# Kernel tuning notes

Measured on AMD Instinct MI355X. Metric: run time of the kernel, lower is better.

## Reference

```python
import jax, jax.numpy as jnp
import numpy as np

B, S, D, H = 4, 2048, 768, 3072

def _layernorm(X):
    # manual LayerNorm: biased variance, no eps, no affine
    mu = jnp.mean(X, axis=2, keepdims=True)
    sigma = jnp.sqrt(jnp.mean(jnp.square(X - mu), axis=2, keepdims=True))
    return (X - mu) / sigma

def setup_inputs() -> dict:
    key = jax.random.key(0)
    ks = jax.random.split(key, 11)
    sc = 0.02
    return {
        "X": jax.random.normal(ks[0], (B, S, D), dtype=jnp.float32),
        "Wq": jax.random.normal(ks[1], (D, D), dtype=jnp.float32) * sc,
        "bq": jnp.zeros((D,), dtype=jnp.float32),
        "Wk": jax.random.normal(ks[2], (D, D), dtype=jnp.float32) * sc,
        "bk": jnp.zeros((D,), dtype=jnp.float32),
        "Wv": jax.random.normal(ks[3], (D, D), dtype=jnp.float32) * sc,
        "bv": jnp.zeros((D,), dtype=jnp.float32),
        "W1": jax.random.normal(ks[4], (D, H), dtype=jnp.float32) * sc,
        "b1": jnp.zeros((H,), dtype=jnp.float32),
        "W2": jax.random.normal(ks[5], (H, D), dtype=jnp.float32) * sc,
        "b2": jnp.zeros((D,), dtype=jnp.float32),
    }

def reference(X, Wq, bq, Wk, bk, Wv, bv, W1, b1, W2, b2):
    dk = jnp.sqrt(jnp.asarray(X.shape[2], dtype=X.dtype))
    Q = X @ Wq + bq
    K = X @ Wk + bk
    V = X @ Wv + bv
    A = jnp.einsum('bqd,bkd->bqk', Q, K)
    # faithful: tril zeroes (not -inf) above-diagonal BEFORE softmax
    A = jnp.tril(A) / dk
    A = jax.nn.softmax(A, axis=2)
    # faithful to einsum 'ijk,ijl->ijl': sum A over k, broadcast onto V
    AV = jnp.sum(A, axis=2, keepdims=True) * V
    X = _layernorm(X + AV)
    F = jax.nn.relu(X @ W1 + b1) @ W2 + b2
    X = _layernorm(X + F)
    return X
```

## Files before the change

kernel.cpp:

```cpp
#include <hip/hip_runtime.h>
#include <hip/hip_bf16.h>
#include <math.h>


typedef __bf16 bf16x8 __attribute__((ext_vector_type(8)));
typedef float f32x4 __attribute__((ext_vector_type(4)));

__device__ inline void gload_lds16(const __hip_bfloat16* g, void* lds) {
  __builtin_amdgcn_global_load_lds(
      (const __attribute__((address_space(1))) void*)g,
      (__attribute__((address_space(3))) void*)lds, 16, 0, 0);
}

__device__ inline float bf2f(unsigned short u) {
  union { unsigned int i; float f; } x;
  x.i = ((unsigned int)u) << 16;
  return x.f;
}

#define BARRIER() asm volatile("s_barrier" ::: "memory")

template <int BNv, int EPI>
__global__ __launch_bounds__(256, 2) void gemm128(
    const __hip_bfloat16* __restrict__ A, const __hip_bfloat16* __restrict__ Bt,
    __hip_bfloat16* __restrict__ C, const float* __restrict__ bias,
    const float* __restrict__ residf, const __hip_bfloat16* __restrict__ residb,
    int M, int N, int K) {
  constexpr int NF = BNv / 32;
  constexpr int BI = BNv / 32;
  constexpr int BS = BNv * 128;
  __shared__ __align__(16) char smem[32768 + 2 * BS];

  const int bid = blockIdx.x;
  const int mB = M / 128;
  const int rowBase = (bid % mB) * 128;
  const int colBase = (bid / mB) * BNv;
  const int nt = K / 64;

  const int wv = threadIdx.x >> 6;
  const int lane = threadIdx.x & 63;
  const int wr = wv >> 1, wc = wv & 1;
  const int l16 = lane & 15, lk = lane >> 4;

  const int rA = lane >> 3;
  const int cSw = ((lane & 7) ^ rA) * 8;
  const __hip_bfloat16* gA = A + (size_t)(rowBase + wv * 32 + rA) * K + cSw;
  const __hip_bfloat16* gB =
      Bt + (size_t)(colBase + wv * 8 * BI + rA) * K + cSw;

  auto STAGE = [&](int kt, int b) {
    const size_t ko = (size_t)kt * 64;
#pragma unroll
    for (int i = 0; i < 4; ++i)
      gload_lds16(gA + (size_t)i * 8 * K + ko,
                  smem + b * 16384 + (wv * 4 + i) * 1024);
#pragma unroll
    for (int i = 0; i < BI; ++i)
      gload_lds16(gB + (size_t)i * 8 * K + ko,
                  smem + 32768 + b * BS + (wv * BI + i) * 1024);
  };

  const int aBase = (wr * 64 + l16) * 128;
  const int bBase = (wc * (BNv / 2) + l16) * 128;
  const int xr = l16 & 7;
  const int cph0 = ((lk) ^ xr) * 16;
  const int cph1 = ((4 + lk) ^ xr) * 16;

  f32x4 acc[4][NF];
#pragma unroll
  for (int m = 0; m < 4; ++m)
#pragma unroll
    for (int n = 0; n < NF; ++n) acc[m][n] = (f32x4){0.f, 0.f, 0.f, 0.f};

  STAGE(0, 0);
  if (nt > 1) {
    STAGE(1, 1);
    if constexpr (BNv == 128)
      asm volatile("s_waitcnt vmcnt(8)" ::: "memory");
    else
      asm volatile("s_waitcnt vmcnt(7)" ::: "memory");
  } else {
    asm volatile("s_waitcnt vmcnt(0)" ::: "memory");
  }
  BARRIER();

  for (int t = 0; t < nt; ++t) {
    const int b = t & 1;
    const char* pa = smem + b * 16384 + aBase;
    const char* pb = smem + 32768 + b * BS + bBase;

    bf16x8 af0[4], af1[4], bf0[NF], bf1[NF];
#pragma unroll
    for (int m = 0; m < 4; ++m) af0[m] = *(const bf16x8*)(pa + m * 2048 + cph0);
#pragma unroll
    for (int n = 0; n < NF; ++n) bf0[n] = *(const bf16x8*)(pb + n * 2048 + cph0);
#pragma unroll
    for (int m = 0; m < 4; ++m) af1[m] = *(const bf16x8*)(pa + m * 2048 + cph1);
#pragma unroll
    for (int n = 0; n < NF; ++n) bf1[n] = *(const bf16x8*)(pb + n * 2048 + cph1);

    if constexpr (NF == 4)
      asm volatile("s_waitcnt lgkmcnt(8)" ::: "memory");
    else
      asm volatile("s_waitcnt lgkmcnt(7)" ::: "memory");
    __builtin_amdgcn_sched_barrier(0);
    __builtin_amdgcn_s_setprio(1);
#pragma unroll
    for (int m = 0; m < 4; ++m)
#pragma unroll
      for (int n = 0; n < NF; ++n)
        acc[m][n] = __builtin_amdgcn_mfma_f32_16x16x32_bf16(af0[m], bf0[n],
                                                            acc[m][n], 0, 0, 0);
    __builtin_amdgcn_s_setprio(0);
    asm volatile("s_waitcnt lgkmcnt(0)" ::: "memory");
    __builtin_amdgcn_sched_barrier(0);
    BARRIER();

    if (t + 2 < nt) STAGE(t + 2, b);

    __builtin_amdgcn_s_setprio(1);
#pragma unroll
    for (int m = 0; m < 4; ++m)
#pragma unroll
      for (int n = 0; n < NF; ++n)
        acc[m][n] = __builtin_amdgcn_mfma_f32_16x16x32_bf16(af1[m], bf1[n],
                                                            acc[m][n], 0, 0, 0);
    __builtin_amdgcn_s_setprio(0);

    if (t + 1 < nt) {
      if (t + 2 < nt) {
        if constexpr (BNv == 128)
          asm volatile("s_waitcnt vmcnt(8)" ::: "memory");
        else
          asm volatile("s_waitcnt vmcnt(7)" ::: "memory");
      } else {
        asm volatile("s_waitcnt vmcnt(0)" ::: "memory");
      }
      BARRIER();
    }
  }

#pragma unroll
  for (int m = 0; m < 4; ++m) {
#pragma unroll
    for (int n = 0; n < NF; ++n) {
#pragma unroll
      for (int j = 0; j < 4; ++j) {
        const int r = rowBase + wr * 64 + m * 16 + lk * 4 + j;
        const int c = colBase + wc * (BNv / 2) + n * 16 + l16;
        const size_t idx = (size_t)r * N + c;
        float v = acc[m][n][j] + bias[c];
        if (EPI == 1) v += residf[idx];
        if (EPI == 2) v = fmaxf(v, 0.f);
        if (EPI == 3) v += __bfloat162float(residb[idx]);
        C[idx] = __float2bfloat16(v);
      }
    }
  }
}

template <bool OUTF>
__global__ __launch_bounds__(256) void ln_simple(
    const __hip_bfloat16* __restrict__ Y, __hip_bfloat16* __restrict__ outb,
    float* __restrict__ outf) {
  const int wave = threadIdx.x >> 6, lane = threadIdx.x & 63;
  const size_t base = ((size_t)blockIdx.x * 4 + wave) * 768;

  float v[12];
  float s = 0.f, q = 0.f;
#pragma unroll
  for (int c = 0; c < 3; ++c) {
    const int col = c * 256 + lane * 4;
    ushort4 a = *reinterpret_cast<const ushort4*>(&Y[base + col]);
    float y0 = bf2f(a.x), y1 = bf2f(a.y), y2 = bf2f(a.z), y3 = bf2f(a.w);
    v[c * 4 + 0] = y0; v[c * 4 + 1] = y1; v[c * 4 + 2] = y2; v[c * 4 + 3] = y3;
    s += y0 + y1 + y2 + y3;
    q += y0 * y0 + y1 * y1 + y2 * y2 + y3 * y3;
  }
#pragma unroll
  for (int off = 32; off; off >>= 1) {
    s += __shfl_xor(s, off);
    q += __shfl_xor(q, off);
  }
  const float mu = s * (1.f / 768.f);
  const float rs = rsqrtf(q * (1.f / 768.f) - mu * mu);
#pragma unroll
  for (int c = 0; c < 3; ++c) {
    const int col = c * 256 + lane * 4;
    if (OUTF) {
      float4 o;
      o.x = (v[c * 4 + 0] - mu) * rs;
      o.y = (v[c * 4 + 1] - mu) * rs;
      o.z = (v[c * 4 + 2] - mu) * rs;
      o.w = (v[c * 4 + 3] - mu) * rs;
      *reinterpret_cast<float4*>(&outf[base + col]) = o;
    } else {
      __hip_bfloat16 h0 = __float2bfloat16((v[c * 4 + 0] - mu) * rs);
      __hip_bfloat16 h1 = __float2bfloat16((v[c * 4 + 1] - mu) * rs);
      __hip_bfloat16 h2 = __float2bfloat16((v[c * 4 + 2] - mu) * rs);
      __hip_bfloat16 h3 = __float2bfloat16((v[c * 4 + 3] - mu) * rs);
      ushort4 o;
      o.x = *reinterpret_cast<unsigned short*>(&h0);
      o.y = *reinterpret_cast<unsigned short*>(&h1);
      o.z = *reinterpret_cast<unsigned short*>(&h2);
      o.w = *reinterpret_cast<unsigned short*>(&h3);
      *reinterpret_cast<ushort4*>(&outb[base + col]) = o;
    }
  }
}

__device__ inline void tc_tile(const float* __restrict__ W,
                               __hip_bfloat16* __restrict__ Wt, int K, int N,
                               int n0, int k0, int t) {
  __shared__ float tile[32][33];
  const int tx = t & 31;
  const int ty = t >> 5;
#pragma unroll
  for (int i = 0; i < 32; i += 8)
    tile[ty + i][tx] = W[(size_t)(k0 + ty + i) * N + n0 + tx];
  __syncthreads();
#pragma unroll
  for (int i = 0; i < 32; i += 8)
    Wt[(size_t)(n0 + ty + i) * K + k0 + tx] = __float2bfloat16(tile[tx][ty + i]);
}

__global__ __launch_bounds__(256) void prep_kernel(
    const float* __restrict__ X, const float* __restrict__ Wv,
    const float* __restrict__ W1, const float* __restrict__ W2,
    __hip_bfloat16* __restrict__ Xb, __hip_bfloat16* __restrict__ Wvt,
    __hip_bfloat16* __restrict__ W1t, __hip_bfloat16* __restrict__ W2t) {
  const int bid = blockIdx.x;
  const int t = threadIdx.x;
  if (bid < 6144) {
    const int i = bid * 256 + t;
    float4 v = reinterpret_cast<const float4*>(X)[i];
    __hip_bfloat16 h0 = __float2bfloat16(v.x), h1 = __float2bfloat16(v.y);
    __hip_bfloat16 h2 = __float2bfloat16(v.z), h3 = __float2bfloat16(v.w);
    ushort4 o;
    o.x = *reinterpret_cast<unsigned short*>(&h0);
    o.y = *reinterpret_cast<unsigned short*>(&h1);
    o.z = *reinterpret_cast<unsigned short*>(&h2);
    o.w = *reinterpret_cast<unsigned short*>(&h3);
    reinterpret_cast<ushort4*>(Xb)[i] = o;
  } else if (bid < 6720) {
    const int idx = bid - 6144;
    tc_tile(Wv, Wvt, 768, 768, (idx % 24) * 32, (idx / 24) * 32, t);
  } else if (bid < 9024) {
    const int idx = bid - 6720;
    tc_tile(W1, W1t, 768, 3072, (idx % 96) * 32, (idx / 96) * 32, t);
  } else {
    const int idx = bid - 9024;
    tc_tile(W2, W2t, 3072, 768, (idx % 24) * 32, (idx / 24) * 32, t);
  }
}

extern "C" void kernel_launch(void* const* d_in, const int* in_sizes, int n_in,
                              void* d_out, int out_size, void* d_ws,
                              size_t ws_size, hipStream_t stream) {
  const float* X = (const float*)d_in[0];
  const float* Wv = (const float*)d_in[5];
  const float* bv = (const float*)d_in[6];
  const float* W1 = (const float*)d_in[7];
  const float* b1 = (const float*)d_in[8];
  const float* W2 = (const float*)d_in[9];
  const float* b2 = (const float*)d_in[10];
  float* out = (float*)d_out;

  const int M = 4 * 2048;
  const int D = 768, H = 3072;

  char* ws = (char*)d_ws;
  __hip_bfloat16* Xb  = (__hip_bfloat16*)(ws);
  __hip_bfloat16* Wvt = (__hip_bfloat16*)(ws + 12582912);
  __hip_bfloat16* W1t = (__hip_bfloat16*)(ws + 13762560);
  __hip_bfloat16* W2t = (__hip_bfloat16*)(ws + 18481152);
  __hip_bfloat16* Yb  = (__hip_bfloat16*)(ws + 23199744);
  __hip_bfloat16* X1b = (__hip_bfloat16*)(ws + 35782656);
  __hip_bfloat16* Gb  = (__hip_bfloat16*)(ws + 48365568);
  __hip_bfloat16* Y2b = Yb;

  prep_kernel<<<11328, 256, 0, stream>>>(X, Wv, W1, W2, Xb, Wvt, W1t, W2t);

  gemm128<96, 1><<<512, 256, 0, stream>>>(Xb, Wvt, Yb, bv, X, nullptr, M, D, D);
  ln_simple<false><<<M / 4, 256, 0, stream>>>(Yb, X1b, nullptr);
  gemm128<128, 2><<<1536, 256, 0, stream>>>(X1b, W1t, Gb, b1, nullptr, nullptr,
                                            M, H, D);
  gemm128<96, 3><<<512, 256, 0, stream>>>(Gb, W2t, Y2b, b2, nullptr, X1b, M, D,
                                          H);
  ln_simple<true><<<M / 4, 256, 0, stream>>>(Y2b, nullptr, out);
}
```

Measured before the change: 125.3 us.

## Switch GEMM mainloop to 4-stage BK=32 ring with register double-buffered fragments

Restructures the bf16 MFMA GEMM mainloop. K tiles shrink from 64 to 32, and LDS becomes a 4-buffer ring with three tiles prefetched ahead. Each iteration loads the next tile's fragments into alternate registers while MFMAs run on the current ones, with one barrier per step instead of two. The aim is to hide global and LDS latency behind compute, at the cost of twice as many iterations and barriers, new swizzle and waitcnt bookkeeping, and an assumption that nt is even and at least 3.

```diff
diff --git a/kernel.cpp b/kernel.cpp
--- a/kernel.cpp
+++ b/kernel.cpp
@@ -27,44 +27,56 @@
     const float* __restrict__ residf, const __hip_bfloat16* __restrict__ residb,
     int M, int N, int K) {
   constexpr int NF = BNv / 32;
-  constexpr int BI = BNv / 32;
-  constexpr int BS = BNv * 128;
-  __shared__ __align__(16) char smem[32768 + 2 * BS];
+  constexpr int BS2 = BNv * 64;
+  __shared__ __align__(16) char smem[32768 + 4 * BS2];
 
   const int bid = blockIdx.x;
   const int mB = M / 128;
   const int rowBase = (bid % mB) * 128;
   const int colBase = (bid / mB) * BNv;
-  const int nt = K / 64;
+  const int nt = K / 32;
 
   const int wv = threadIdx.x >> 6;
   const int lane = threadIdx.x & 63;
   const int wr = wv >> 1, wc = wv & 1;
   const int l16 = lane & 15, lk = lane >> 4;
-
-  const int rA = lane >> 3;
-  const int cSw = ((lane & 7) ^ rA) * 8;
-  const __hip_bfloat16* gA = A + (size_t)(rowBase + wv * 32 + rA) * K + cSw;
-  const __hip_bfloat16* gB =
-      Bt + (size_t)(colBase + wv * 8 * BI + rA) * K + cSw;
+  const bool hasB = (BNv == 128) || (wv < 3);
+  const bool SW4 = hasB;
+
+  const int sr = lane >> 2;
+  const int scol = ((lane & 3) ^ ((sr >> 1) & 3)) * 8;
+  const __hip_bfloat16* gA = A + (size_t)(rowBase + wv * 32 + sr) * K + scol;
+  const __hip_bfloat16* gB = Bt + (size_t)(colBase + wv * 32 + sr) * K + scol;
 
   auto STAGE = [&](int kt, int b) {
-    const size_t ko = (size_t)kt * 64;
-#pragma unroll
-    for (int i = 0; i < 4; ++i)
-      gload_lds16(gA + (size_t)i * 8 * K + ko,
-                  smem + b * 16384 + (wv * 4 + i) * 1024);
-#pragma unroll
-    for (int i = 0; i < BI; ++i)
-      gload_lds16(gB + (size_t)i * 8 * K + ko,
-                  smem + 32768 + b * BS + (wv * BI + i) * 1024);
+    const size_t ko = (size_t)kt * 32;
+#pragma unroll
+    for (int i = 0; i < 2; ++i)
+      gload_lds16(gA + (size_t)i * 16 * K + ko,
+                  smem + b * 8192 + (wv * 2 + i) * 1024);
+    if (hasB) {
+#pragma unroll
+      for (int i = 0; i < 2; ++i)
+        gload_lds16(gB + (size_t)i * 16 * K + ko,
+                    smem + 32768 + b * BS2 + (wv * 2 + i) * 1024);
+    }
   };
 
-  const int aBase = (wr * 64 + l16) * 128;
-  const int bBase = (wc * (BNv / 2) + l16) * 128;
-  const int xr = l16 & 7;
-  const int cph0 = ((lk) ^ xr) * 16;
-  const int cph1 = ((4 + lk) ^ xr) * 16;
+  auto WAITSTAGE = [&](int t) {
+    if (t + 3 < nt) {
+      if (SW4) asm volatile("s_waitcnt vmcnt(8)" ::: "memory");
+      else     asm volatile("s_waitcnt vmcnt(4)" ::: "memory");
+    } else if (t + 2 < nt) {
+      if (SW4) asm volatile("s_waitcnt vmcnt(4)" ::: "memory");
+      else     asm volatile("s_waitcnt vmcnt(2)" ::: "memory");
+    } else {
+      asm volatile("s_waitcnt vmcnt(0)" ::: "memory");
+    }
+  };
+
+  const int aByte = (wr * 64 + l16) * 64;
+  const int bByte = (wc * (BNv / 2) + l16) * 64;
+  const int cph = (lk ^ ((l16 >> 1) & 3)) * 16;
 
   f32x4 acc[4][NF];
 #pragma unroll
@@ -72,73 +84,59 @@
 #pragma unroll
     for (int n = 0; n < NF; ++n) acc[m][n] = (f32x4){0.f, 0.f, 0.f, 0.f};
 
+  bf16x8 a0[4], b0[NF], a1[4], b1[NF];
+
   STAGE(0, 0);
-  if (nt > 1) {
-    STAGE(1, 1);
-    if constexpr (BNv == 128)
-      asm volatile("s_waitcnt vmcnt(8)" ::: "memory");
-    else
-      asm volatile("s_waitcnt vmcnt(7)" ::: "memory");
-  } else {
-    asm volatile("s_waitcnt vmcnt(0)" ::: "memory");
-  }
+  STAGE(1, 1);
+  STAGE(2, 2);
+  if (SW4) asm volatile("s_waitcnt vmcnt(8)" ::: "memory");
+  else     asm volatile("s_waitcnt vmcnt(4)" ::: "memory");
   BARRIER();
-
-  for (int t = 0; t < nt; ++t) {
-    const int b = t & 1;
-    const char* pa = smem + b * 16384 + aBase;
-    const char* pb = smem + 32768 + b * BS + bBase;
-
-    bf16x8 af0[4], af1[4], bf0[NF], bf1[NF];
-#pragma unroll
-    for (int m = 0; m < 4; ++m) af0[m] = *(const bf16x8*)(pa + m * 2048 + cph0);
-#pragma unroll
-    for (int n = 0; n < NF; ++n) bf0[n] = *(const bf16x8*)(pb + n * 2048 + cph0);
-#pragma unroll
-    for (int m = 0; m < 4; ++m) af1[m] = *(const bf16x8*)(pa + m * 2048 + cph1);
-#pragma unroll
-    for (int n = 0; n < NF; ++n) bf1[n] = *(const bf16x8*)(pb + n * 2048 + cph1);
-
-    if constexpr (NF == 4)
-      asm volatile("s_waitcnt lgkmcnt(8)" ::: "memory");
-    else
-      asm volatile("s_waitcnt lgkmcnt(7)" ::: "memory");
-    __builtin_amdgcn_sched_barrier(0);
-    __builtin_amdgcn_s_setprio(1);
-#pragma unroll
-    for (int m = 0; m < 4; ++m)
-#pragma unroll
-      for (int n = 0; n < NF; ++n)
-        acc[m][n] = __builtin_amdgcn_mfma_f32_16x16x32_bf16(af0[m], bf0[n],
-                                                            acc[m][n], 0, 0, 0);
-    __builtin_amdgcn_s_setprio(0);
-    asm volatile("s_waitcnt lgkmcnt(0)" ::: "memory");
-    __builtin_amdgcn_sched_barrier(0);
-    BARRIER();
-
-    if (t + 2 < nt) STAGE(t + 2, b);
-
-    __builtin_amdgcn_s_setprio(1);
-#pragma unroll
-    for (int m = 0; m < 4; ++m)
-#pragma unroll
-      for (int n = 0; n < NF; ++n)
-        acc[m][n] = __builtin_amdgcn_mfma_f32_16x16x32_bf16(af1[m], bf1[n],
-                                                            acc[m][n], 0, 0, 0);
-    __builtin_amdgcn_s_setprio(0);
-
-    if (t + 1 < nt) {
-      if (t + 2 < nt) {
-        if constexpr (BNv == 128)
-          asm volatile("s_waitcnt vmcnt(8)" ::: "memory");
-        else
-          asm volatile("s_waitcnt vmcnt(7)" ::: "memory");
-      } else {
-        asm volatile("s_waitcnt vmcnt(0)" ::: "memory");
-      }
-      BARRIER();
-    }
-  }
+  {
+    const char* pa = smem + aByte;
+    const char* pb = smem + 32768 + bByte;
+#pragma unroll
+    for (int m = 0; m < 4; ++m) a0[m] = *(const bf16x8*)(pa + m * 1024 + cph);
+#pragma unroll
+    for (int n = 0; n < NF; ++n) b0[n] = *(const bf16x8*)(pb + n * 1024 + cph);
+  }
+
+#define ITER(T, CA, CB, NA, NB)                                               \
+  {                                                                           \
+    const int t_ = (T);                                                       \
+    asm volatile("s_waitcnt lgkmcnt(0)" ::: "memory");                        \
+    __builtin_amdgcn_sched_barrier(0);                                        \
+    if (t_ + 3 < nt) STAGE(t_ + 3, (t_ + 3) & 3);                             \
+    WAITSTAGE(t_);                                                            \
+    BARRIER();                                                                \
+    if (t_ + 1 < nt) {                                                        \
+      const char* pa = smem + ((t_ + 1) & 3) * 8192 + aByte;                  \
+      const char* pb = smem + 32768 + ((t_ + 1) & 3) * BS2 + bByte;           \
+      _Pragma("unroll")                                                       \
+      for (int m = 0; m < 4; ++m)                                             \
+        NA[m] = *(const bf16x8*)(pa + m * 1024 + cph);                        \
+      _Pragma("unroll")                                                       \
+      for (int n = 0; n < NF; ++n)                                            \
+        NB[n] = *(const bf16x8*)(pb + n * 1024 + cph);                        \
+    }                                                                         \
+    __builtin_amdgcn_sched_barrier(0);                                        \
+    __builtin_amdgcn_s_setprio(1);                                            \
+    _Pragma("unroll")                                                         \
+    for (int m = 0; m < 4; ++m) {                                             \
+      _Pragma("unroll")                                                       \
+      for (int n = 0; n < NF; ++n)                                            \
+        acc[m][n] = __builtin_amdgcn_mfma_f32_16x16x32_bf16(CA[m], CB[n],     \
+                                                            acc[m][n], 0, 0,  \
+                                                            0);               \
+    }                                                                         \
+    __builtin_amdgcn_s_setprio(0);                                            \
+  }
+
+  for (int t = 0; t < nt; t += 2) {
+    ITER(t, a0, b0, a1, b1);
+    ITER(t + 1, a1, b1, a0, b0);
+  }
+#undef ITER
 
 #pragma unroll
   for (int m = 0; m < 4; ++m) {
```

Measured after the change: 148.7 us. 18.7% more time.

## Use 256x256 ping-pong GEMM for FFN with split-K second GEMM fused into final LN

Applied to the files above, without the earlier changes.

Adds a 512-thread 256x256-tile bf16 MFMA GEMM with a four-slot LDS pipeline and interleaved phase barriers. The FFN up-projection runs on it, and the down-projection runs on it as a split-K=2 kernel writing two bf16 partials. A new final LayerNorm kernel sums the partials, residual and bias. The larger tiles aim to raise data reuse and MFMA utilisation and to fill the GPU better for N=768. The cost is extra partial-sum traffic and an extra rounding of the partials to bf16. Workspace offsets are reshuffled so Gb and Yb alias.

```diff
diff --git a/kernel.cpp b/kernel.cpp
--- a/kernel.cpp
+++ b/kernel.cpp
@@ -19,6 +19,165 @@
 }
 
 #define BARRIER() asm volatile("s_barrier" ::: "memory")
+
+template <int EPI>
+__global__ __launch_bounds__(512, 2) void gemm256(
+    const __hip_bfloat16* __restrict__ A, const __hip_bfloat16* __restrict__ Bt,
+    __hip_bfloat16* __restrict__ C, const float* __restrict__ bias,
+    int M, int N, int K, int Ksub, int mB, int nB) {
+  __shared__ __align__(16) char smem[131072];
+
+  const int bid = blockIdx.x;
+  const int bpz = mB * nB;
+  const int z = bid / bpz;
+  const int rem = bid % bpz;
+  const int rowBase = (rem % mB) * 256;
+  const int colBase = (rem / mB) * 256;
+  const int kBase = z * Ksub;
+  const int nt = Ksub / 64;
+
+  const int wv = threadIdx.x >> 6;
+  const int lane = threadIdx.x & 63;
+  const int wr = wv >> 2;
+  const int wc = wv & 3;
+  const int l16 = lane & 15, lk = lane >> 4;
+
+  const int srow = lane >> 3;
+  const int scol = ((lane & 7) ^ srow) * 8;
+  const __hip_bfloat16* gA =
+      A + (size_t)(rowBase + srow) * K + kBase + scol;
+  const __hip_bfloat16* gB =
+      Bt + (size_t)(colBase + srow) * K + kBase + scol;
+
+  auto SA = [&](int tau, int h) {
+    if (tau >= 2 && tau < nt) {
+      const int slot = (2 * tau + h) & 3;
+#pragma unroll
+      for (int i = 0; i < 2; ++i)
+        gload_lds16(gA + (size_t)(128 * h + 8 * (2 * wv + i)) * K +
+                        (size_t)tau * 64,
+                    smem + slot * 16384 + (wv * 2 + i) * 1024);
+    }
+  };
+  auto SB = [&](int tau, int h) {
+    if (tau >= 2 && tau < nt) {
+      const int slot = (2 * tau + h) & 3;
+#pragma unroll
+      for (int i = 0; i < 2; ++i)
+        gload_lds16(gB + (size_t)(128 * h + 8 * (2 * wv + i)) * K +
+                        (size_t)tau * 64,
+                    smem + 65536 + slot * 16384 + (wv * 2 + i) * 1024);
+    }
+  };
+
+  const int aOff = l16 * 128;
+  const int bOff = (wc & 1) * 8192 + l16 * 128;
+  const int cph0 = ((lk) ^ (l16 & 7)) * 16;
+  const int cph1 = ((4 + lk) ^ (l16 & 7)) * 16;
+
+  f32x4 acc[8][4];
+#pragma unroll
+  for (int m = 0; m < 8; ++m)
+#pragma unroll
+    for (int n = 0; n < 4; ++n) acc[m][n] = (f32x4){0.f, 0.f, 0.f, 0.f};
+
+  bf16x8 bq0[4], bq1[4];
+
+  {
+#pragma unroll
+    for (int tt = 0; tt < 2; ++tt) {
+      const int s0 = 2 * tt;
+#pragma unroll
+      for (int h = 0; h < 2; ++h)
+#pragma unroll
+        for (int i = 0; i < 2; ++i)
+          gload_lds16(gA + (size_t)(128 * h + 8 * (2 * wv + i)) * K +
+                          (size_t)tt * 64,
+                      smem + (s0 + h) * 16384 + (wv * 2 + i) * 1024);
+#pragma unroll
+      for (int h = 0; h < 2; ++h)
+#pragma unroll
+        for (int i = 0; i < 2; ++i)
+          gload_lds16(gB + (size_t)(128 * h + 8 * (2 * wv + i)) * K +
+                          (size_t)tt * 64,
+                      smem + 65536 + (s0 + h) * 16384 + (wv * 2 + i) * 1024);
+    }
+    asm volatile("s_waitcnt vmcnt(8)" ::: "memory");
+    BARRIER();
+  }
+
+#define PH(T, MH, READB, BQ, CPH, STG, VM)                                   \
+  {                                                                          \
+    const char* pa_ = smem + (((2 * (T) + wr) & 3) * 16384) + aOff;          \
+    bf16x8 af_[4];                                                           \
+    _Pragma("unroll") for (int m_ = 0; m_ < 4; ++m_) af_[m_] =               \
+        *(const bf16x8*)(pa_ + ((MH)*4 + m_) * 2048 + (CPH));                \
+    if (READB) {                                                             \
+      const char* pb_ =                                                      \
+          smem + 65536 + (((2 * (T) + (wc >> 1)) & 3) * 16384) + bOff;       \
+      _Pragma("unroll") for (int n_ = 0; n_ < 4; ++n_) BQ[n_] =              \
+          *(const bf16x8*)(pb_ + n_ * 2048 + (CPH));                         \
+    }                                                                        \
+    STG;                                                                     \
+    BARRIER();                                                               \
+    asm volatile("s_waitcnt lgkmcnt(0)" ::: "memory");                       \
+    __builtin_amdgcn_sched_barrier(0);                                       \
+    __builtin_amdgcn_s_setprio(1);                                           \
+    _Pragma("unroll") for (int m_ = 0; m_ < 4; ++m_) {                       \
+      _Pragma("unroll") for (int n_ = 0; n_ < 4; ++n_) acc[(MH)*4 + m_][n_] =\
+          __builtin_amdgcn_mfma_f32_16x16x32_bf16(af_[m_], BQ[n_],           \
+                                                  acc[(MH)*4 + m_][n_], 0,   \
+                                                  0, 0);                     \
+    }                                                                        \
+    __builtin_amdgcn_s_setprio(0);                                           \
+    VM;                                                                      \
+    BARRIER();                                                               \
+  }
+
+  const int iters = nt / 2;
+  for (int i = 0; i < iters; ++i) {
+    const int e = 2 * i, o = 2 * i + 1;
+    PH(e, 0, 1, bq0, cph0, SB(o, 1), (void)0);
+    PH(e, 1, 0, bq0, cph0, SA(o, 0), (void)0);
+    PH(e, 0, 1, bq1, cph1, SA(o, 1), (void)0);
+    if (e + 2 < nt) {
+      PH(e, 1, 0, bq1, cph1, SB(e + 2, 0),
+         asm volatile("s_waitcnt vmcnt(2)" ::: "memory"));
+    } else {
+      PH(e, 1, 0, bq1, cph1, (void)0,
+         asm volatile("s_waitcnt vmcnt(0)" ::: "memory"));
+    }
+    if (e + 2 < nt) {
+      PH(o, 0, 1, bq0, cph0, SB(e + 2, 1), (void)0);
+      PH(o, 1, 0, bq0, cph0, SA(e + 2, 0), (void)0);
+      PH(o, 0, 1, bq1, cph1, SA(e + 2, 1), (void)0);
+      PH(o, 1, 0, bq1, cph1, SB(o + 2, 0),
+         asm volatile("s_waitcnt vmcnt(2)" ::: "memory"));
+    } else {
+      PH(o, 0, 1, bq0, cph0, (void)0, (void)0);
+      PH(o, 1, 0, bq0, cph0, (void)0, (void)0);
+      PH(o, 0, 1, bq1, cph1, (void)0, (void)0);
+      PH(o, 1, 0, bq1, cph1, (void)0, (void)0);
+    }
+  }
+#undef PH
+
+  __hip_bfloat16* Cz = C + (size_t)z * M * N;
+#pragma unroll
+  for (int m = 0; m < 8; ++m) {
+#pragma unroll
+    for (int n = 0; n < 4; ++n) {
+#pragma unroll
+      for (int j = 0; j < 4; ++j) {
+        const int r = rowBase + wr * 128 + m * 16 + lk * 4 + j;
+        const int c = colBase + wc * 64 + n * 16 + l16;
+        float v = acc[m][n][j];
+        if (EPI == 2) v = fmaxf(v + bias[c], 0.f);
+        Cz[(size_t)r * N + c] = __float2bfloat16(v);
+      }
+    }
+  }
+}
 
 template <int BNv, int EPI>
 __global__ __launch_bounds__(256, 2) void gemm128(
@@ -206,6 +365,49 @@
       o.w = *reinterpret_cast<unsigned short*>(&h3);
       *reinterpret_cast<ushort4*>(&outb[base + col]) = o;
     }
+  }
+}
+
+__global__ __launch_bounds__(256) void ln_fuse2_final(
+    const __hip_bfloat16* __restrict__ P0, const __hip_bfloat16* __restrict__ P1,
+    const __hip_bfloat16* __restrict__ residb, const float* __restrict__ bias,
+    float* __restrict__ outf) {
+  const int wave = threadIdx.x >> 6, lane = threadIdx.x & 63;
+  const size_t base = ((size_t)blockIdx.x * 4 + wave) * 768;
+
+  float v[12];
+  float s = 0.f, q = 0.f;
+#pragma unroll
+  for (int c = 0; c < 3; ++c) {
+    const int col = c * 256 + lane * 4;
+    ushort4 a = *reinterpret_cast<const ushort4*>(&P0[base + col]);
+    ushort4 b = *reinterpret_cast<const ushort4*>(&P1[base + col]);
+    ushort4 rb = *reinterpret_cast<const ushort4*>(&residb[base + col]);
+    float4 bs = *reinterpret_cast<const float4*>(&bias[col]);
+    float y0 = bf2f(a.x) + bf2f(b.x) + bf2f(rb.x) + bs.x;
+    float y1 = bf2f(a.y) + bf2f(b.y) + bf2f(rb.y) + bs.y;
+    float y2 = bf2f(a.z) + bf2f(b.z) + bf2f(rb.z) + bs.z;
+    float y3 = bf2f(a.w) + bf2f(b.w) + bf2f(rb.w) + bs.w;
+    v[c * 4 + 0] = y0; v[c * 4 + 1] = y1; v[c * 4 + 2] = y2; v[c * 4 + 3] = y3;
+    s += y0 + y1 + y2 + y3;
+    q += y0 * y0 + y1 * y1 + y2 * y2 + y3 * y3;
+  }
+#pragma unroll
+  for (int off = 32; off; off >>= 1) {
+    s += __shfl_xor(s, off);
+    q += __shfl_xor(q, off);
+  }
+  const float mu = s * (1.f / 768.f);
+  const float rs = rsqrtf(q * (1.f / 768.f) - mu * mu);
+#pragma unroll
+  for (int c = 0; c < 3; ++c) {
+    const int col = c * 256 + lane * 4;
+    float4 o;
+    o.x = (v[c * 4 + 0] - mu) * rs;
+    o.y = (v[c * 4 + 1] - mu) * rs;
+    o.z = (v[c * 4 + 2] - mu) * rs;
+    o.w = (v[c * 4 + 3] - mu) * rs;
+    *reinterpret_cast<float4*>(&outf[base + col]) = o;
   }
 }
 
@@ -273,19 +475,19 @@
   __hip_bfloat16* Xb  = (__hip_bfloat16*)(ws);
   __hip_bfloat16* Wvt = (__hip_bfloat16*)(ws + 12582912);
   __hip_bfloat16* W1t = (__hip_bfloat16*)(ws + 13762560);
-  __hip_bfloat16* W2t = (__hip_bfloat16*)(ws + 18481152);
-  __hip_bfloat16* Yb  = (__hip_bfloat16*)(ws + 23199744);
-  __hip_bfloat16* X1b = (__hip_bfloat16*)(ws + 35782656);
-  __hip_bfloat16* Gb  = (__hip_bfloat16*)(ws + 48365568);
-  __hip_bfloat16* Y2b = Yb;
+  __hip_bfloat16* W2t = (__hip_bfloat16*)(ws + 25165824);
+  __hip_bfloat16* X1b = (__hip_bfloat16*)(ws + 29884416);
+  __hip_bfloat16* Gb  = (__hip_bfloat16*)(ws + 42467328);
+  __hip_bfloat16* Yb  = (__hip_bfloat16*)(ws + 42467328);
+  __hip_bfloat16* P3  = (__hip_bfloat16*)(ws);
 
   prep_kernel<<<11328, 256, 0, stream>>>(X, Wv, W1, W2, Xb, Wvt, W1t, W2t);
 
   gemm128<96, 1><<<512, 256, 0, stream>>>(Xb, Wvt, Yb, bv, X, nullptr, M, D, D);
   ln_simple<false><<<M / 4, 256, 0, stream>>>(Yb, X1b, nullptr);
-  gemm128<128, 2><<<1536, 256, 0, stream>>>(X1b, W1t, Gb, b1, nullptr, nullptr,
-                                            M, H, D);
-  gemm128<96, 3><<<512, 256, 0, stream>>>(Gb, W2t, Y2b, b2, nullptr, X1b, M, D,
-                                          H);
-  ln_simple<true><<<M / 4, 256, 0, stream>>>(Y2b, nullptr, out);
-}
+  gemm256<2><<<384, 512, 0, stream>>>(X1b, W1t, Gb, b1, M, H, D, D, 32, 12);
+  gemm256<0><<<192, 512, 0, stream>>>(Gb, W2t, P3, nullptr, M, D, H, H / 2,
+                                      32, 3);
+  ln_fuse2_final<<<M / 4, 256, 0, stream>>>(P3, P3 + (size_t)M * D, X1b, b2,
+                                            out);
+}
```

Result: slower. 423.1 us (+237.8%).
